# Optimization experiments

Measured on AMD Instinct MI355X. Metric: run time of the kernel, lower is better.

The kernel has to match this reference:

```python
import jax, jax.numpy as jnp
import numpy as np

S, D, H, DI, DV, DFF = 2048, 1024, 16, 64, 64, 4096


def _xavier(k, shape):
    fan_in, fan_out = shape[-2], shape[-1]
    lim = float(np.sqrt(6.0 / (fan_in + fan_out)))
    return jax.random.uniform(k, shape, jnp.float32, -lim, lim)


def setup_inputs() -> dict:
    key = jax.random.key(0)
    ks = jax.random.split(key, 8)
    input_vecs = jax.random.normal(ks[0], (S, D), jnp.float32)
    WQs = _xavier(ks[1], (H, D, DI))
    WKs = _xavier(ks[2], (H, D, DI))
    WVs = _xavier(ks[3], (H, D, DV))
    WO_w = _xavier(ks[4], (D, H * DV))   # torch Linear weight [out, in]
    WO_b = jnp.zeros((D,), jnp.float32)
    FF1_w = _xavier(ks[5], (DFF, D))
    FF1_b = jnp.zeros((DFF,), jnp.float32)
    FF2_w = _xavier(ks[6], (D, DFF))
    FF2_b = jnp.zeros((D,), jnp.float32)
    return dict(input_vecs=input_vecs, WQs=WQs, WKs=WKs, WVs=WVs,
                WO_w=WO_w, WO_b=WO_b, FF1_w=FF1_w, FF1_b=FF1_b,
                FF2_w=FF2_w, FF2_b=FF2_b)


def reference(input_vecs, WQs, WKs, WVs, WO_w, WO_b, FF1_w, FF1_b, FF2_w, FF2_b):
    h, _, di = WQs.shape
    s = input_vecs.shape[0]
    # per-head projections: [h, s, di/dv]
    Q = jnp.einsum('sd,hde->hse', input_vecs, WQs)
    K = jnp.einsum('sd,hde->hse', input_vecs, WKs)
    V = jnp.einsum('sd,hdv->hsv', input_vecs, WVs)
    scores = jnp.einsum('hse,hte->hst', Q, K) / jnp.sqrt(jnp.float32(di))
    # ALiBi bias: slope_h = (2^{-8/H})^h for h = 1..H; bias = -max(0, i-j)*slope
    idx = jnp.arange(s)
    delta = idx[:, None] - idx[None, :]               # [s, s], i - j
    slopes = (2.0 ** (-8.0 / h)) ** jnp.arange(1, h + 1, dtype=jnp.float32)
    bias = -jnp.maximum(delta, 0).astype(jnp.float32) * slopes[:, None, None]
    causal_mask = jnp.where(delta < 0, -jnp.inf, 0.0)  # -inf above diagonal
    SA = jax.nn.softmax(scores + bias + causal_mask, axis=-1)  # [h, s, s]
    z = jnp.einsum('hst,htv->hsv', SA, V)
    # hstack over heads == transpose to [s, h, dv] then flatten
    zconcat = jnp.transpose(z, (1, 0, 2)).reshape(s, -1)
    attouts = input_vecs + zconcat @ WO_w.T + WO_b
    output_vecs = attouts + jax.nn.relu(attouts @ FF1_w.T + FF1_b) @ FF2_w.T + FF2_b
    return SA, output_vecs
```

## Files before the change

kernel.cpp:

```cpp
#include <hip/hip_runtime.h>
#include <hip/hip_bf16.h>

typedef __hip_bfloat16 bf16;
typedef short v8s __attribute__((ext_vector_type(8)));
typedef float f32x4 __attribute__((ext_vector_type(4)));

static constexpr int S = 2048, D = 1024, H = 16, DFF = 4096;

__device__ __forceinline__ bf16  f2b(float x) { return __float2bfloat16(x); }
__device__ __forceinline__ float b2f(bf16 x)  { return __bfloat162float(x); }

__device__ __forceinline__ void gl2lds16(const void* g, void* l) {
    __builtin_amdgcn_global_load_lds(
        (const __attribute__((address_space(1))) unsigned int*)g,
        (__attribute__((address_space(3))) unsigned int*)l, 16, 0, 0);
}

__global__ __launch_bounds__(256)
void prep(const float* __restrict__ X, const float* __restrict__ WO,
          const float* __restrict__ F1, const float* __restrict__ F2,
          bf16* __restrict__ Xb, bf16* __restrict__ WOb,
          bf16* __restrict__ F1b, bf16* __restrict__ F2b,
          const float* __restrict__ WQ, const float* __restrict__ WK,
          const float* __restrict__ WV, bf16* __restrict__ Wcat)
{
    __shared__ float t[64][65];
    const int bid = blockIdx.x, tid = threadIdx.x;
    if (bid < 16384) {
        const float* src; bf16* dst; int n4;
        switch (bid >> 12) {
            case 0:  src = X;  dst = Xb;  n4 = S * D / 4;   break;
            case 1:  src = WO; dst = WOb; n4 = D * D / 4;   break;
            case 2:  src = F1; dst = F1b; n4 = DFF * D / 4; break;
            default: src = F2; dst = F2b; n4 = D * DFF / 4; break;
        }
        const int i = (bid & 4095) * 256 + tid;
        if (i < n4) {
            const float4 v = ((const float4*)src)[i];
            bf16* p = dst + (size_t)i * 4;
            p[0] = f2b(v.x); p[1] = f2b(v.y); p[2] = f2b(v.z); p[3] = f2b(v.w);
        }
    } else {
        const int rem = bid - 16384;
        const int d0 = (rem & 15) * 64, h = (rem >> 4) & 15, sel = rem >> 8;
        const float* W = (sel == 0) ? WQ : (sel == 1) ? WK : WV;
        for (int idx = tid; idx < 4096; idx += 256) {
            const int d = idx >> 6, e = idx & 63;
            t[d][e] = W[((size_t)h * D + d0 + d) * 64 + e];
        }
        __syncthreads();
        for (int idx = tid; idx < 4096; idx += 256) {
            const int e = idx >> 6, d = idx & 63;
            Wcat[(size_t)(sel * 1024 + h * 64 + e) * D + d0 + d] = f2b(t[d][e]);
        }
    }
}

template<int EPI>
__global__ __launch_bounds__(256)
void gemm_nt(const bf16* __restrict__ A, const bf16* __restrict__ B,
             int M, int N, int Kd, int Kstride,
             const float* __restrict__ bias, const float* __restrict__ res_f,
             float* __restrict__ out_f, bf16* __restrict__ out_h,
             bf16* __restrict__ Qb, bf16* __restrict__ Kb, bf16* __restrict__ Vt)
{
    __shared__ bf16 sA[128 * 32];
    __shared__ bf16 sB[128 * 32];
    const int tid = threadIdx.x;
    const int lane = tid & 63, quad = lane >> 4, l15 = lane & 15;
    const int wave = tid >> 6, wm = wave >> 1, wn = wave & 1;
    const size_t m0 = (size_t)blockIdx.x * 128, n0 = (size_t)blockIdx.y * 128;
    const int koff = (EPI == 4) ? blockIdx.z * Kd : 0;
    const int trow = tid >> 2, tcol = (tid & 3) * 8;

    const bf16* pA = A + (m0 + trow) * (size_t)Kstride + koff + tcol;
    const bf16* pB = B + (n0 + trow) * (size_t)Kstride + koff + tcol;
    bf16* lA = sA + tid * 8;
    bf16* lB = sB + tid * 8;

    f32x4 acc[4][4] = {};

    for (int k0 = 0; k0 < Kd; k0 += 32) {
        gl2lds16(pA + k0, lA);
        gl2lds16(pA + 64 * (size_t)Kstride + k0, lA + 2048);
        gl2lds16(pB + k0, lB);
        gl2lds16(pB + 64 * (size_t)Kstride + k0, lB + 2048);
        __syncthreads();
        v8s af[4], bfr[4];
        #pragma unroll
        for (int t = 0; t < 4; ++t) {
            af[t]  = *(const v8s*)(sA + (wm * 64 + t * 16 + l15) * 32 + quad * 8);
            bfr[t] = *(const v8s*)(sB + (wn * 64 + t * 16 + l15) * 32 + quad * 8);
        }
        #pragma unroll
        for (int i = 0; i < 4; ++i)
            #pragma unroll
            for (int j = 0; j < 4; ++j)
                acc[i][j] = __builtin_amdgcn_mfma_f32_16x16x32_bf16(af[i], bfr[j], acc[i][j], 0, 0, 0);
        __syncthreads();
    }

    #pragma unroll
    for (int i = 0; i < 4; ++i) {
        const size_t mbase = m0 + wm * 64 + i * 16 + quad * 4;
        #pragma unroll
        for (int j = 0; j < 4; ++j) {
            const size_t n = n0 + wn * 64 + j * 16 + l15;
            if constexpr (EPI == 0) {
                const int sel = (int)(n >> 10), hh = (int)((n >> 6) & 15), e = (int)(n & 63);
                if (sel == 2) {
                    bf16* p = Vt + ((size_t)hh * 64 + e) * S + mbase;
                    p[0] = f2b(acc[i][j][0]); p[1] = f2b(acc[i][j][1]);
                    p[2] = f2b(acc[i][j][2]); p[3] = f2b(acc[i][j][3]);
                } else {
                    const float sc = (sel == 0) ? 0.125f : 1.0f;
                    bf16* p = ((sel == 0) ? Qb : Kb) + ((size_t)hh * S + mbase) * 64 + e;
                    p[0]   = f2b(acc[i][j][0] * sc);
                    p[64]  = f2b(acc[i][j][1] * sc);
                    p[128] = f2b(acc[i][j][2] * sc);
                    p[192] = f2b(acc[i][j][3] * sc);
                }
            } else if constexpr (EPI == 4) {
                float* po = out_f + (size_t)blockIdx.z * (size_t)M * N;
                #pragma unroll
                for (int r = 0; r < 4; ++r)
                    po[(mbase + r) * (size_t)N + n] = acc[i][j][r];
            }
        }
    }
}

template<int EPI>
__global__ __launch_bounds__(512, 2)
void gemm256(const bf16* __restrict__ A, const bf16* __restrict__ B,
             int M, int N, int Kd, int Kstride,
             const float* __restrict__ bias,
             float* __restrict__ out_f, bf16* __restrict__ out_h)
{
    __shared__ __attribute__((aligned(16))) bf16 sA[2][256 * 64];
    __shared__ __attribute__((aligned(16))) bf16 sB[2][256 * 64];
    const int tid = threadIdx.x;
    const int lane = tid & 63, wave = tid >> 6;
    const int quad = lane >> 4, l15 = lane & 15;
    const int wm = wave >> 2, wn = wave & 3;
    const size_t m0 = (size_t)blockIdx.x * 256, n0 = (size_t)blockIdx.y * 256;
    const int koff = (EPI == 4) ? blockIdx.z * Kd : 0;
    const int NT = Kd / 64;
    const int srow = lane >> 3, schunk = lane & 7;

    f32x4 acc[8][4] = {};

#define STAGE_A(buf, tt, h)                                                    \
    {                                                                          \
        const int k0s = koff + (tt) * 64;                                      \
        _Pragma("unroll")                                                      \
        for (int l = 0; l < 2; ++l) {                                          \
            const int c = wave * 2 + l;                                        \
            const int r0 = (c >> 3) * 128 + (h) * 64 + (c & 7) * 8;            \
            const int rr = r0 + srow;                                          \
            const int sc = schunk ^ (rr & 7);                                  \
            const bf16* gp = A + (m0 + (size_t)rr) * (size_t)Kstride           \
                               + k0s + sc * 8;                                 \
            gl2lds16(gp, &buf[r0 * 64] + lane * 8);                            \
        }                                                                      \
    }

#define STAGE_B(buf, tt, h)                                                    \
    {                                                                          \
        const int k0s = koff + (tt) * 64;                                      \
        _Pragma("unroll")                                                      \
        for (int l = 0; l < 2; ++l) {                                          \
            const int c = wave * 2 + l;                                        \
            const int r0 = (c >> 2) * 64 + (h) * 32 + (c & 3) * 8;             \
            const int rr = r0 + srow;                                          \
            const int sc = schunk ^ (rr & 7);                                  \
            const bf16* gp = B + (n0 + (size_t)rr) * (size_t)Kstride           \
                               + k0s + sc * 8;                                 \
            gl2lds16(gp, &buf[r0 * 64] + lane * 8);                            \
        }                                                                      \
    }

#define PHASE(bufA, bufB, mh, nh, STAGE_STMT, WAIT_STMT)                       \
    {                                                                          \
        v8s af[4][2], bv[2][2];                                                \
        _Pragma("unroll")                                                      \
        for (int f = 0; f < 4; ++f)                                            \
            _Pragma("unroll")                                                  \
            for (int ks = 0; ks < 2; ++ks) {                                   \
                const int r = wm * 128 + (mh) * 64 + f * 16 + l15;             \
                const int byt = (r * 128 + ks * 64 + quad * 16) ^ ((r & 7) << 4); \
                af[f][ks] = *(const v8s*)((const char*)(bufA) + byt);          \
            }                                                                  \
        _Pragma("unroll")                                                      \
        for (int g = 0; g < 2; ++g)                                            \
            _Pragma("unroll")                                                  \
            for (int ks = 0; ks < 2; ++ks) {                                   \
                const int r = wn * 64 + (nh) * 32 + g * 16 + l15;              \
                const int byt = (r * 128 + ks * 64 + quad * 16) ^ ((r & 7) << 4); \
                bv[g][ks] = *(const v8s*)((const char*)(bufB) + byt);          \
            }                                                                  \
        STAGE_STMT;                                                            \
        __builtin_amdgcn_s_barrier();                                          \
        __builtin_amdgcn_s_setprio(1);                                         \
        _Pragma("unroll")                                                      \
        for (int ks = 0; ks < 2; ++ks)                                         \
            _Pragma("unroll")                                                  \
            for (int f = 0; f < 4; ++f)                                        \
                _Pragma("unroll")                                              \
                for (int g = 0; g < 2; ++g)                                    \
                    acc[(mh) * 4 + f][(nh) * 2 + g] =                          \
                        __builtin_amdgcn_mfma_f32_16x16x32_bf16(               \
                            af[f][ks], bv[g][ks],                              \
                            acc[(mh) * 4 + f][(nh) * 2 + g], 0, 0, 0);         \
        __builtin_amdgcn_s_setprio(0);                                         \
        WAIT_STMT;                                                             \
        __builtin_amdgcn_s_barrier();                                          \
    }

    bf16* a0 = sA[0]; bf16* a1 = sA[1];
    bf16* b0 = sB[0]; bf16* b1 = sB[1];

    STAGE_A(a0, 0, 0); STAGE_A(a0, 0, 1);
    STAGE_B(b0, 0, 0); STAGE_B(b0, 0, 1);
    STAGE_A(a1, 1, 0); STAGE_B(b1, 1, 0);
    asm volatile("s_waitcnt vmcnt(4)" ::: "memory");
    __builtin_amdgcn_s_barrier();

    for (int t = 0; t < NT; ++t) {
        bf16* cA = (t & 1) ? a1 : a0; bf16* cB = (t & 1) ? b1 : b0;
        bf16* nA = (t & 1) ? a0 : a1; bf16* nB = (t & 1) ? b0 : b1;
        const bool s1 = (t + 1 < NT), s2 = (t + 2 < NT);
        PHASE(cA, cB, 0, 0, { if (s1) STAGE_A(nA, t + 1, 1); }, {});
        PHASE(cA, cB, 0, 1, { if (s1) STAGE_B(nB, t + 1, 1); }, {});
        PHASE(cA, cB, 1, 0, { if (s2) STAGE_A(cA, t + 2, 0); }, {});
        PHASE(cA, cB, 1, 1, { if (s2) STAGE_B(cB, t + 2, 0); },
              { if (s2) { asm volatile("s_waitcnt vmcnt(4)" ::: "memory"); }
                else    { asm volatile("s_waitcnt vmcnt(0)" ::: "memory"); } });
    }
#undef PHASE
#undef STAGE_A
#undef STAGE_B

    #pragma unroll
    for (int mf = 0; mf < 8; ++mf) {
        const size_t mr = m0 + wm * 128 + mf * 16 + quad * 4;
        #pragma unroll
        for (int nf = 0; nf < 4; ++nf) {
            const size_t n = n0 + wn * 64 + nf * 16 + l15;
            if constexpr (EPI == 2) {
                const float bval = bias[n];
                #pragma unroll
                for (int r = 0; r < 4; ++r)
                    out_h[(mr + r) * (size_t)N + n] =
                        f2b(fmaxf(acc[mf][nf][r] + bval, 0.f));
            } else {
                float* po = out_f + (size_t)blockIdx.z * ((size_t)M * N);
                #pragma unroll
                for (int r = 0; r < 4; ++r)
                    po[(mr + r) * (size_t)N + n] = acc[mf][nf][r];
            }
        }
    }
}

__global__ __launch_bounds__(256)
void wo_combine(const float* __restrict__ p0, const float* __restrict__ p1,
                const float* __restrict__ bias, const float* __restrict__ X,
                float* __restrict__ attf, bf16* __restrict__ atth)
{
    const int i = blockIdx.x * 256 + threadIdx.x;
    const float4 a = ((const float4*)p0)[i];
    const float4 b = ((const float4*)p1)[i];
    const float4 x = ((const float4*)X)[i];
    const float4 bs = ((const float4*)bias)[i & (D / 4 - 1)];
    float4 o;
    o.x = a.x + b.x + x.x + bs.x;
    o.y = a.y + b.y + x.y + bs.y;
    o.z = a.z + b.z + x.z + bs.z;
    o.w = a.w + b.w + x.w + bs.w;
    ((float4*)attf)[i] = o;
    bf16* ph = atth + (size_t)i * 4;
    ph[0] = f2b(o.x); ph[1] = f2b(o.y); ph[2] = f2b(o.z); ph[3] = f2b(o.w);
}

__global__ __launch_bounds__(256)
void ff2_combine4(const float* __restrict__ p0, const float* __restrict__ p1,
                  const float* __restrict__ p2, const float* __restrict__ p3,
                  const float* __restrict__ bias, const float* __restrict__ attf,
                  float* __restrict__ out2)
{
    const int i = blockIdx.x * 256 + threadIdx.x;
    const float4 a = ((const float4*)p0)[i];
    const float4 b = ((const float4*)p1)[i];
    const float4 c = ((const float4*)p2)[i];
    const float4 d = ((const float4*)p3)[i];
    const float4 r = ((const float4*)attf)[i];
    const float4 bs = ((const float4*)bias)[i & (D / 4 - 1)];
    float4 o;
    o.x = a.x + b.x + c.x + d.x + r.x + bs.x;
    o.y = a.y + b.y + c.y + d.y + r.y + bs.y;
    o.z = a.z + b.z + c.z + d.z + r.z + bs.z;
    o.w = a.w + b.w + c.w + d.w + r.w + bs.w;
    ((float4*)out2)[i] = o;
}

__global__ __launch_bounds__(512)
void attn_kernel(const bf16* __restrict__ Qb, const bf16* __restrict__ Kb,
                 const bf16* __restrict__ Vt, float* __restrict__ SA,
                 bf16* __restrict__ zf)
{
    constexpr int EST = 2056;
    __shared__ bf16 ebuf[16 * EST];
    __shared__ float wsum[8][16];
    __shared__ float inv16[16];
    __shared__ float pvacc[8][16][16];

    const int bi = (int)gridDim.x - 1 - (int)blockIdx.x;
    const int h = blockIdx.y;
    const int i0 = bi * 16;
    const int tid = threadIdx.x, wave = tid >> 6, lane = tid & 63;
    const int quad = lane >> 4, l15 = lane & 15;
    const int ntiles = bi + 1;
    const float slope = exp2f(-0.5f * (float)(h + 1));

    if (tid < 256) {
        const int r = tid >> 4, c = ntiles * 16 + (tid & 15);
        if (c < EST) ebuf[r * EST + c] = f2b(0.f);
    }

    const bf16* Qrow = Qb + ((size_t)h * S + i0 + l15) * 64;
    const v8s qf0 = *(const v8s*)(Qrow + quad * 8);
    const v8s qf1 = *(const v8s*)(Qrow + 32 + quad * 8);

    const bf16* Kh = Kb + (size_t)h * S * 64;
    float esum[4] = {0.f, 0.f, 0.f, 0.f};
    {
        int jt = wave;
        v8s kf0 = {}, kf1 = {};
        if (jt < ntiles) {
            const bf16* Krow = Kh + (size_t)(jt * 16 + l15) * 64;
            kf0 = *(const v8s*)(Krow + quad * 8);
            kf1 = *(const v8s*)(Krow + 32 + quad * 8);
        }
        while (jt < ntiles) {
            const int jn = jt + 8;
            v8s nf0 = kf0, nf1 = kf1;
            if (jn < ntiles) {
                const bf16* Krow = Kh + (size_t)(jn * 16 + l15) * 64;
                nf0 = *(const v8s*)(Krow + quad * 8);
                nf1 = *(const v8s*)(Krow + 32 + quad * 8);
            }
            f32x4 c = {0.f, 0.f, 0.f, 0.f};
            c = __builtin_amdgcn_mfma_f32_16x16x32_bf16(qf0, kf0, c, 0, 0, 0);
            c = __builtin_amdgcn_mfma_f32_16x16x32_bf16(qf1, kf1, c, 0, 0, 0);
            const int j = jt * 16 + l15;
            #pragma unroll
            for (int r = 0; r < 4; ++r) {
                const int i = i0 + quad * 4 + r;
                float e = 0.f;
                if (j <= i) e = __expf(c[r] - (float)(i - j) * slope);
                const bf16 eb = f2b(e);
                ebuf[(quad * 4 + r) * EST + j] = eb;
                esum[r] += b2f(eb);
            }
            kf0 = nf0; kf1 = nf1; jt = jn;
        }
    }
    #pragma unroll
    for (int r = 0; r < 4; ++r) {
        float v = esum[r];
        v += __shfl_xor(v, 1); v += __shfl_xor(v, 2);
        v += __shfl_xor(v, 4); v += __shfl_xor(v, 8);
        if (l15 == 0) wsum[wave][quad * 4 + r] = v;
    }
    __syncthreads();
    if (tid < 16) {
        float s = 0.f;
        #pragma unroll
        for (int w = 0; w < 8; ++w) s += wsum[w][tid];
        inv16[tid] = 1.f / s;
    }
    __syncthreads();

    {
        const int c4 = tid;
        const int nst4 = ((i0 + 15) >> 2) + 1;
        if (c4 < nst4) {
            const int col = c4 * 4;
            float* SAb = SA + ((size_t)h * S + i0) * S;
            #pragma unroll 4
            for (int row = 0; row < 16; ++row) {
                const int i = i0 + row;
                if (col <= i) {
                    const float iv = inv16[row];
                    const bf16* er = ebuf + row * EST + col;
                    float4 o;
                    o.x = b2f(er[0]) * iv;
                    o.y = (col + 1 <= i) ? b2f(er[1]) * iv : 0.f;
                    o.z = (col + 2 <= i) ? b2f(er[2]) * iv : 0.f;
                    o.w = (col + 3 <= i) ? b2f(er[3]) * iv : 0.f;
                    ((float4*)(SAb + (size_t)row * S))[c4] = o;
                }
            }
        }
    }

    const int nc = (bi + 2) >> 1;
    const int vt = wave & 3, jh = wave >> 2;
    const bf16* Vrow = Vt + ((size_t)h * 64 + vt * 16 + l15) * (size_t)S;
    f32x4 oc = {0.f, 0.f, 0.f, 0.f};
    {
        int ch = jh;
        v8s vf = {};
        if (ch < nc) vf = *(const v8s*)(Vrow + ch * 32 + quad * 8);
        while (ch < nc) {
            const int cn = ch + 2;
            v8s vn = vf;
            if (cn < nc) vn = *(const v8s*)(Vrow + cn * 32 + quad * 8);
            const v8s pf = *(const v8s*)(ebuf + l15 * EST + ch * 32 + quad * 8);
            oc = __builtin_amdgcn_mfma_f32_16x16x32_bf16(pf, vf, oc, 0, 0, 0);
            vf = vn; ch = cn;
        }
    }
    #pragma unroll
    for (int r = 0; r < 4; ++r)
        pvacc[wave][quad * 4 + r][l15] = oc[r];
    __syncthreads();
    for (int idx = tid; idx < 1024; idx += 512) {
        const int v4 = idx >> 8, rem = idx & 255, row = rem >> 4, col = rem & 15;
        const float z = (pvacc[v4][row][col] + pvacc[v4 + 4][row][col]) * inv16[row];
        zf[(size_t)(i0 + row) * (H * 64) + h * 64 + v4 * 16 + col] = f2b(z);
    }
}

extern "C" void kernel_launch(void* const* d_in, const int* in_sizes, int n_in,
                              void* d_out, int out_size, void* d_ws, size_t ws_size,
                              hipStream_t stream)
{
    const float* X     = (const float*)d_in[0];
    const float* WQs   = (const float*)d_in[1];
    const float* WKs   = (const float*)d_in[2];
    const float* WVs   = (const float*)d_in[3];
    const float* WO_w  = (const float*)d_in[4];
    const float* WO_b  = (const float*)d_in[5];
    const float* FF1_w = (const float*)d_in[6];
    const float* FF1_b = (const float*)d_in[7];
    const float* FF2_w = (const float*)d_in[8];
    const float* FF2_b = (const float*)d_in[9];

    float* SA   = (float*)d_out;
    float* out2 = SA + (size_t)H * S * S;

    char* ws = (char*)d_ws;
    const size_t MB = 1u << 20;
    bf16*  FF1b = (bf16*)(ws);
    bf16*  FF2b = (bf16*)(ws + 8 * MB);
    bf16*  Xb   = (bf16*)(ws + 16 * MB);
    bf16*  Wcat = (bf16*)(ws + 20 * MB);
    bf16*  WOb  = (bf16*)(ws + 26 * MB);
    bf16*  zf   = (bf16*)(ws + 28 * MB);
    bf16*  Qb   = (bf16*)(ws + 32 * MB);
    bf16*  Kb   = (bf16*)(ws + 36 * MB);
    bf16*  Vt   = (bf16*)(ws + 40 * MB);
    float* attf = (float*)(ws + 44 * MB);
    bf16*  atth = (bf16*)(ws + 52 * MB);
    bf16*  y1   = (bf16*)(ws + 56 * MB);
    float* pW   = (float*)(ws + 72 * MB);

    const size_t SD = (size_t)S * D;

    prep<<<dim3(16384 + 768), 256, 0, stream>>>(X, WO_w, FF1_w, FF2_w,
        Xb, WOb, FF1b, FF2b, WQs, WKs, WVs, Wcat);
    gemm_nt<0><<<dim3(16, 24), 256, 0, stream>>>(Xb, Wcat, S, 3072, D, D,
        nullptr, nullptr, nullptr, nullptr, Qb, Kb, Vt);
    attn_kernel<<<dim3(S / 16, H), 512, 0, stream>>>(Qb, Kb, Vt, SA, zf);
    gemm_nt<4><<<dim3(16, 8, 2), 256, 0, stream>>>(zf, WOb, S, D, D / 2, D,
        nullptr, nullptr, pW, nullptr, nullptr, nullptr, nullptr);
    wo_combine<<<dim3(S * D / 4 / 256), 256, 0, stream>>>(
        pW, pW + SD, WO_b, X, attf, atth);
    gemm256<2><<<dim3(8, 16), 512, 0, stream>>>(atth, FF1b, S, DFF, D, D,
        FF1_b, nullptr, y1);
    gemm256<4><<<dim3(8, 4, 4), 512, 0, stream>>>(y1, FF2b, S, D, DFF / 4, DFF,
        nullptr, pW, nullptr);
    ff2_combine4<<<dim3(S * D / 4 / 256), 256, 0, stream>>>(
        pW, pW + SD, pW + 2 * SD, pW + 3 * SD, FF2_b, attf, out2);
}
```

Before: 526.6 us.

## Shrink GEMM tile to 128x256 and route QKV projection through pipelined kernel

The 256x256 pipelined GEMM becomes a 128x256 variant (gemm128n), with staging, fragment loads, accumulators and waitcnt counts reduced to match. FF1 and FF2 now launch twice as many blocks, which should give better CU occupancy across the 256 CUs. The QKV projection also moves from the simpler 128x128 gemm_nt to this double-buffered kernel, keeping its scatter epilogue for the Q/K/V layouts. The trade-off is less operand reuse per block and more total global/LDS traffic.

After: 506.6 us. 1.04x faster.

```diff
diff --git a/kernel.cpp b/kernel.cpp
--- a/kernel.cpp
+++ b/kernel.cpp
@@ -60,9 +60,7 @@
 __global__ __launch_bounds__(256)
 void gemm_nt(const bf16* __restrict__ A, const bf16* __restrict__ B,
              int M, int N, int Kd, int Kstride,
-             const float* __restrict__ bias, const float* __restrict__ res_f,
-             float* __restrict__ out_f, bf16* __restrict__ out_h,
-             bf16* __restrict__ Qb, bf16* __restrict__ Kb, bf16* __restrict__ Vt)
+             float* __restrict__ out_f)
 {
     __shared__ bf16 sA[128 * 32];
     __shared__ bf16 sB[128 * 32];
@@ -70,7 +68,7 @@
     const int lane = tid & 63, quad = lane >> 4, l15 = lane & 15;
     const int wave = tid >> 6, wm = wave >> 1, wn = wave & 1;
     const size_t m0 = (size_t)blockIdx.x * 128, n0 = (size_t)blockIdx.y * 128;
-    const int koff = (EPI == 4) ? blockIdx.z * Kd : 0;
+    const int koff = blockIdx.z * Kd;
     const int trow = tid >> 2, tcol = (tid & 3) * 8;
 
     const bf16* pA = A + (m0 + trow) * (size_t)Kstride + koff + tcol;
@@ -106,63 +104,45 @@
         #pragma unroll
         for (int j = 0; j < 4; ++j) {
             const size_t n = n0 + wn * 64 + j * 16 + l15;
-            if constexpr (EPI == 0) {
-                const int sel = (int)(n >> 10), hh = (int)((n >> 6) & 15), e = (int)(n & 63);
-                if (sel == 2) {
-                    bf16* p = Vt + ((size_t)hh * 64 + e) * S + mbase;
-                    p[0] = f2b(acc[i][j][0]); p[1] = f2b(acc[i][j][1]);
-                    p[2] = f2b(acc[i][j][2]); p[3] = f2b(acc[i][j][3]);
-                } else {
-                    const float sc = (sel == 0) ? 0.125f : 1.0f;
-                    bf16* p = ((sel == 0) ? Qb : Kb) + ((size_t)hh * S + mbase) * 64 + e;
-                    p[0]   = f2b(acc[i][j][0] * sc);
-                    p[64]  = f2b(acc[i][j][1] * sc);
-                    p[128] = f2b(acc[i][j][2] * sc);
-                    p[192] = f2b(acc[i][j][3] * sc);
-                }
-            } else if constexpr (EPI == 4) {
-                float* po = out_f + (size_t)blockIdx.z * (size_t)M * N;
-                #pragma unroll
-                for (int r = 0; r < 4; ++r)
-                    po[(mbase + r) * (size_t)N + n] = acc[i][j][r];
-            }
+            float* po = out_f + (size_t)blockIdx.z * (size_t)M * N;
+            #pragma unroll
+            for (int r = 0; r < 4; ++r)
+                po[(mbase + r) * (size_t)N + n] = acc[i][j][r];
         }
     }
 }
 
 template<int EPI>
 __global__ __launch_bounds__(512, 2)
-void gemm256(const bf16* __restrict__ A, const bf16* __restrict__ B,
-             int M, int N, int Kd, int Kstride,
-             const float* __restrict__ bias,
-             float* __restrict__ out_f, bf16* __restrict__ out_h)
-{
-    __shared__ __attribute__((aligned(16))) bf16 sA[2][256 * 64];
+void gemm128n(const bf16* __restrict__ A, const bf16* __restrict__ B,
+              int M, int N, int Kd, int Kstride,
+              const float* __restrict__ bias,
+              float* __restrict__ out_f, bf16* __restrict__ out_h,
+              bf16* __restrict__ Qb, bf16* __restrict__ Kb, bf16* __restrict__ Vt)
+{
+    __shared__ __attribute__((aligned(16))) bf16 sA[2][128 * 64];
     __shared__ __attribute__((aligned(16))) bf16 sB[2][256 * 64];
     const int tid = threadIdx.x;
     const int lane = tid & 63, wave = tid >> 6;
     const int quad = lane >> 4, l15 = lane & 15;
     const int wm = wave >> 2, wn = wave & 3;
-    const size_t m0 = (size_t)blockIdx.x * 256, n0 = (size_t)blockIdx.y * 256;
+    const size_t m0 = (size_t)blockIdx.x * 128, n0 = (size_t)blockIdx.y * 256;
     const int koff = (EPI == 4) ? blockIdx.z * Kd : 0;
     const int NT = Kd / 64;
     const int srow = lane >> 3, schunk = lane & 7;
 
-    f32x4 acc[8][4] = {};
+    f32x4 acc[4][4] = {};
 
 #define STAGE_A(buf, tt, h)                                                    \
     {                                                                          \
         const int k0s = koff + (tt) * 64;                                      \
-        _Pragma("unroll")                                                      \
-        for (int l = 0; l < 2; ++l) {                                          \
-            const int c = wave * 2 + l;                                        \
-            const int r0 = (c >> 3) * 128 + (h) * 64 + (c & 7) * 8;            \
-            const int rr = r0 + srow;                                          \
-            const int sc = schunk ^ (rr & 7);                                  \
-            const bf16* gp = A + (m0 + (size_t)rr) * (size_t)Kstride           \
-                               + k0s + sc * 8;                                 \
-            gl2lds16(gp, &buf[r0 * 64] + lane * 8);                            \
-        }                                                                      \
+        const int c = wave;                                                    \
+        const int r0 = (c >> 2) * 64 + (h) * 32 + (c & 3) * 8;                 \
+        const int rr = r0 + srow;                                              \
+        const int sc = schunk ^ (rr & 7);                                      \
+        const bf16* gp = A + (m0 + (size_t)rr) * (size_t)Kstride               \
+                           + k0s + sc * 8;                                     \
+        gl2lds16(gp, &buf[r0 * 64] + lane * 8);                                \
     }
 
 #define STAGE_B(buf, tt, h)                                                    \
@@ -182,12 +162,12 @@
 
 #define PHASE(bufA, bufB, mh, nh, STAGE_STMT, WAIT_STMT)                       \
     {                                                                          \
-        v8s af[4][2], bv[2][2];                                                \
+        v8s af[2][2], bv[2][2];                                                \
         _Pragma("unroll")                                                      \
-        for (int f = 0; f < 4; ++f)                                            \
+        for (int f = 0; f < 2; ++f)                                            \
             _Pragma("unroll")                                                  \
             for (int ks = 0; ks < 2; ++ks) {                                   \
-                const int r = wm * 128 + (mh) * 64 + f * 16 + l15;             \
+                const int r = wm * 64 + (mh) * 32 + f * 16 + l15;              \
                 const int byt = (r * 128 + ks * 64 + quad * 16) ^ ((r & 7) << 4); \
                 af[f][ks] = *(const v8s*)((const char*)(bufA) + byt);          \
             }                                                                  \
@@ -205,13 +185,13 @@
         _Pragma("unroll")                                                      \
         for (int ks = 0; ks < 2; ++ks)                                         \
             _Pragma("unroll")                                                  \
-            for (int f = 0; f < 4; ++f)                                        \
+            for (int f = 0; f < 2; ++f)                                        \
                 _Pragma("unroll")                                              \
                 for (int g = 0; g < 2; ++g)                                    \
-                    acc[(mh) * 4 + f][(nh) * 2 + g] =                          \
+                    acc[(mh) * 2 + f][(nh) * 2 + g] =                          \
                         __builtin_amdgcn_mfma_f32_16x16x32_bf16(               \
                             af[f][ks], bv[g][ks],                              \
-                            acc[(mh) * 4 + f][(nh) * 2 + g], 0, 0, 0);         \
+                            acc[(mh) * 2 + f][(nh) * 2 + g], 0, 0, 0);         \
         __builtin_amdgcn_s_setprio(0);                                         \
         WAIT_STMT;                                                             \
         __builtin_amdgcn_s_barrier();                                          \
@@ -223,7 +203,7 @@
     STAGE_A(a0, 0, 0); STAGE_A(a0, 0, 1);
     STAGE_B(b0, 0, 0); STAGE_B(b0, 0, 1);
     STAGE_A(a1, 1, 0); STAGE_B(b1, 1, 0);
-    asm volatile("s_waitcnt vmcnt(4)" ::: "memory");
+    asm volatile("s_waitcnt vmcnt(3)" ::: "memory");
     __builtin_amdgcn_s_barrier();
 
     for (int t = 0; t < NT; ++t) {
@@ -234,7 +214,7 @@
         PHASE(cA, cB, 0, 1, { if (s1) STAGE_B(nB, t + 1, 1); }, {});
         PHASE(cA, cB, 1, 0, { if (s2) STAGE_A(cA, t + 2, 0); }, {});
         PHASE(cA, cB, 1, 1, { if (s2) STAGE_B(cB, t + 2, 0); },
-              { if (s2) { asm volatile("s_waitcnt vmcnt(4)" ::: "memory"); }
+              { if (s2) { asm volatile("s_waitcnt vmcnt(3)" ::: "memory"); }
                 else    { asm volatile("s_waitcnt vmcnt(0)" ::: "memory"); } });
     }
 #undef PHASE
@@ -242,22 +222,36 @@
 #undef STAGE_B
 
     #pragma unroll
-    for (int mf = 0; mf < 8; ++mf) {
-        const size_t mr = m0 + wm * 128 + mf * 16 + quad * 4;
+    for (int mf = 0; mf < 4; ++mf) {
+        const size_t mbase = m0 + wm * 64 + mf * 16 + quad * 4;
         #pragma unroll
         for (int nf = 0; nf < 4; ++nf) {
             const size_t n = n0 + wn * 64 + nf * 16 + l15;
-            if constexpr (EPI == 2) {
+            if constexpr (EPI == 0) {
+                const int sel = (int)(n >> 10), hh = (int)((n >> 6) & 15), e = (int)(n & 63);
+                if (sel == 2) {
+                    bf16* p = Vt + ((size_t)hh * 64 + e) * S + mbase;
+                    p[0] = f2b(acc[mf][nf][0]); p[1] = f2b(acc[mf][nf][1]);
+                    p[2] = f2b(acc[mf][nf][2]); p[3] = f2b(acc[mf][nf][3]);
+                } else {
+                    const float sc = (sel == 0) ? 0.125f : 1.0f;
+                    bf16* p = ((sel == 0) ? Qb : Kb) + ((size_t)hh * S + mbase) * 64 + e;
+                    p[0]   = f2b(acc[mf][nf][0] * sc);
+                    p[64]  = f2b(acc[mf][nf][1] * sc);
+                    p[128] = f2b(acc[mf][nf][2] * sc);
+                    p[192] = f2b(acc[mf][nf][3] * sc);
+                }
+            } else if constexpr (EPI == 2) {
                 const float bval = bias[n];
                 #pragma unroll
                 for (int r = 0; r < 4; ++r)
-                    out_h[(mr + r) * (size_t)N + n] =
+                    out_h[(mbase + r) * (size_t)N + n] =
                         f2b(fmaxf(acc[mf][nf][r] + bval, 0.f));
             } else {
                 float* po = out_f + (size_t)blockIdx.z * ((size_t)M * N);
                 #pragma unroll
                 for (int r = 0; r < 4; ++r)
-                    po[(mr + r) * (size_t)N + n] = acc[mf][nf][r];
+                    po[(mbase + r) * (size_t)N + n] = acc[mf][nf][r];
             }
         }
     }
@@ -471,17 +465,16 @@
 
     prep<<<dim3(16384 + 768), 256, 0, stream>>>(X, WO_w, FF1_w, FF2_w,
         Xb, WOb, FF1b, FF2b, WQs, WKs, WVs, Wcat);
-    gemm_nt<0><<<dim3(16, 24), 256, 0, stream>>>(Xb, Wcat, S, 3072, D, D,
-        nullptr, nullptr, nullptr, nullptr, Qb, Kb, Vt);
+    gemm128n<0><<<dim3(16, 12), 512, 0, stream>>>(Xb, Wcat, S, 3072, D, D,
+        nullptr, nullptr, nullptr, Qb, Kb, Vt);
     attn_kernel<<<dim3(S / 16, H), 512, 0, stream>>>(Qb, Kb, Vt, SA, zf);
-    gemm_nt<4><<<dim3(16, 8, 2), 256, 0, stream>>>(zf, WOb, S, D, D / 2, D,
-        nullptr, nullptr, pW, nullptr, nullptr, nullptr, nullptr);
+    gemm_nt<4><<<dim3(16, 8, 2), 256, 0, stream>>>(zf, WOb, S, D, D / 2, D, pW);
     wo_combine<<<dim3(S * D / 4 / 256), 256, 0, stream>>>(
         pW, pW + SD, WO_b, X, attf, atth);
-    gemm256<2><<<dim3(8, 16), 512, 0, stream>>>(atth, FF1b, S, DFF, D, D,
-        FF1_b, nullptr, y1);
-    gemm256<4><<<dim3(8, 4, 4), 512, 0, stream>>>(y1, FF2b, S, D, DFF / 4, DFF,
-        nullptr, pW, nullptr);
+    gemm128n<2><<<dim3(16, 16), 512, 0, stream>>>(atth, FF1b, S, DFF, D, D,
+        FF1_b, nullptr, y1, nullptr, nullptr, nullptr);
+    gemm128n<4><<<dim3(16, 4, 4), 512, 0, stream>>>(y1, FF2b, S, D, DFF / 4, DFF,
+        nullptr, pW, nullptr, nullptr, nullptr, nullptr);
     ff2_combine4<<<dim3(S * D / 4 / 256), 256, 0, stream>>>(
         pW, pW + SD, pW + 2 * SD, pW + 3 * SD, FF2_b, attf, out2);
 }
```
